# Performance work log

Measured on AMD Instinct MI355X. Metric: run time of the kernel, lower is better.

The kernel has to match this reference:

```python
import jax, jax.numpy as jnp
import numpy as np
from jax import lax

KS = 3
N = KS ** 3  # 27 kernel taps


def setup_inputs() -> dict:
    key = jax.random.key(0)
    k1, k2, k3 = jax.random.split(key, 3)
    B, Cin, Cout, D, H, W = 1, 32, 32, 32, 48, 48
    x = jax.random.normal(k1, (B, Cin, D, H, W), jnp.float32)
    # offset conv: 81 = 3*27 output channels, no bias (nn.Conv3d(..., bias=False))
    w_off = jax.random.normal(k2, (3 * N, Cin, KS, KS, KS), jnp.float32) * 0.01
    # deform conv kernel (bias defaults to None -> no bias)
    w_def = jax.random.normal(k3, (Cout, Cin, KS, KS, KS), jnp.float32) / np.sqrt(Cin * N)
    return {"x": x, "w_off": w_off, "w_def": w_def}


def _deform_block(x, w_off, w_def):
    B, C, D, H, W = x.shape
    dt = x.dtype

    # standard dense offset conv, padding=1
    offsets = lax.conv_general_dilated(
        x, w_off, (1, 1, 1), [(1, 1), (1, 1), (1, 1)],
        dimension_numbers=("NCDHW", "OIDHW", "NCDHW"))
    off = jnp.transpose(offsets, (0, 2, 3, 4, 1))  # (B,D,H,W,3N)
    od, oh, ow = off[..., :N], off[..., N:2 * N], off[..., 2 * N:]

    # zero-pad input (ConstantPad3d(1))
    xp = jnp.pad(x, ((0, 0), (0, 0), (1, 1), (1, 1), (1, 1)))
    Dp, Hp, Wp = D + 2, H + 2, W + 2

    # p_n: kernel grid offsets in (kd,kh,kw) row-major order, matching conv-weight layout
    r = jnp.arange(-(KS // 2), KS // 2 + 1, dtype=dt)
    pn = jnp.stack(jnp.meshgrid(r, r, r, indexing="ij"), 0).reshape(3, N)
    # p_0: centers in padded coordinates (1..D etc.)
    p0d = jnp.arange(1, D + 1, dtype=dt)[:, None, None, None]
    p0h = jnp.arange(1, H + 1, dtype=dt)[None, :, None, None]
    p0w = jnp.arange(1, W + 1, dtype=dt)[None, None, :, None]

    pd = p0d + pn[0] + od  # (B,D,H,W,N) sampling coords
    ph = p0h + pn[1] + oh
    pw = p0w + pn[2] + ow

    # integer corners (detached in original)
    fd = lax.stop_gradient(jnp.floor(pd))
    fh = lax.stop_gradient(jnp.floor(ph))
    fw = lax.stop_gradient(jnp.floor(pw))
    qd0 = jnp.clip(fd, 0, Dp - 1); qd1 = jnp.clip(fd + 1, 0, Dp - 1)
    qh0 = jnp.clip(fh, 0, Hp - 1); qh1 = jnp.clip(fh + 1, 0, Hp - 1)
    qw0 = jnp.clip(fw, 0, Wp - 1); qw1 = jnp.clip(fw + 1, 0, Wp - 1)

    # clip p to valid range (as in reference impl)
    pd = jnp.clip(pd, 0, Dp - 1)
    ph = jnp.clip(ph, 0, Hp - 1)
    pw = jnp.clip(pw, 0, Wp - 1)

    # trilinear weights per axis: g = 1 - |q - p|
    gd0 = 1 + (qd0 - pd); gd1 = 1 - (qd1 - pd)
    gh0 = 1 + (qh0 - ph); gh1 = 1 - (qh1 - ph)
    gw0 = 1 + (qw0 - pw); gw1 = 1 - (qw1 - pw)

    xf = xp.reshape(B, C, Dp * Hp * Wp)

    def gather(idd, ihh, iww):
        lin = ((idd.astype(jnp.int32) * Hp + ihh.astype(jnp.int32)) * Wp
               + iww.astype(jnp.int32)).reshape(B, 1, -1)
        v = jnp.take_along_axis(xf, jnp.broadcast_to(lin, (B, C, lin.shape[-1])), axis=2)
        return v.reshape(B, C, D, H, W, N)

    x_off = jnp.zeros((B, C, D, H, W, N), dt)
    for gd, idd in ((gd0, qd0), (gd1, qd1)):
        for gh, ihh in ((gh0, qh0), (gh1, qh1)):
            for gw, iww in ((gw0, qw0), (gw1, qw1)):
                x_off = x_off + (gd * gh * gw)[:, None] * gather(idd, ihh, iww)

    # stride-ks conv over reshaped x_offset == weighted sum over the N taps
    Cout = w_def.shape[0]
    out = jnp.einsum("bcdhwn,ocn->bodhw", x_off, w_def.reshape(Cout, C, N))
    return out


def reference(x, w_off, w_def):
    return _deform_block(x, w_off, w_def)
```

## Files before the change

### kernel.cpp

```cpp
#include <hip/hip_runtime.h>

typedef __attribute__((ext_vector_type(8))) short  short8;
typedef __attribute__((ext_vector_type(4))) float  f32x4;
typedef __attribute__((ext_vector_type(2))) float  f32x2;

#define CIN 32
#define COUT 32
#define DD 32
#define HH 48
#define WW 48
#define NTAP 27
#define SPATIAL (DD*HH*WW)

#define BP2_ELEMS (27*6*64*8)
#define OFF_WPK   ((size_t)BP2_ELEMS*2)
#define WPK_ELEMS (27*2*64*8)
#define OFF_XT    (OFF_WPK + (size_t)WPK_ELEMS*2)

#define SB0() __builtin_amdgcn_sched_barrier(0)

__device__ __forceinline__ unsigned short f2bf(float f) {
    union { float f; unsigned u; } v; v.f = f;
    unsigned r = v.u + 0x7FFFu + ((v.u >> 16) & 1u);
    return (unsigned short)(r >> 16);
}
__device__ __forceinline__ float bitsf(unsigned u) {
    union { unsigned u; float f; } v; v.u = u; return v.f;
}

__global__ __launch_bounds__(256) void wprep2_kernel(
        const float* __restrict__ w_off, unsigned short* __restrict__ Bp2)
{
    int i = blockIdx.x * 256 + threadIdx.x;
    if (i >= BP2_ELEMS) return;
    int e    = i & 7;
    int lane = (i >> 3) & 63;
    int j    = (i >> 9) % 6;
    int n    = i / (512 * 6);
    int col = lane & 15, kg = lane >> 4;
    int oc = j * 16 + col, c = kg * 8 + e;
    float v = (oc < 81) ? w_off[((size_t)oc * CIN + c) * NTAP + n] : 0.f;
    Bp2[i] = f2bf(v);
}

__global__ __launch_bounds__(256) void wdefprep_kernel(
        const float* __restrict__ w_def, unsigned short* __restrict__ wpk)
{
    int i = blockIdx.x * 256 + threadIdx.x;
    if (i >= WPK_ELEMS) return;
    int e    = i & 7;
    int lane = (i >> 3) & 63;
    int half = (i >> 9) & 1;
    int n    = i >> 10;
    int kg = lane >> 4, col = lane & 15;
    int c  = kg * 8 + e, oc = half * 16 + col;
    wpk[i] = f2bf(w_def[((size_t)oc * CIN + c) * NTAP + n]);
}

__global__ __launch_bounds__(256) void xtrans_kernel(
        const float* __restrict__ x, unsigned short* __restrict__ xT)
{
    __shared__ float t[CIN][65];
    const int p0 = blockIdx.x * 64;
    const int tid = threadIdx.x;
    const int tx = tid & 63, ty = tid >> 6;
    #pragma unroll
    for (int k = 0; k < 8; ++k) {
        int c = ty + k * 4;
        t[c][tx] = x[(size_t)c * SPATIAL + p0 + tx];
    }
    __syncthreads();
    const int pl = tid >> 2, cg = (tid & 3) * 8;
    short8 v;
    #pragma unroll
    for (int i = 0; i < 8; ++i) v[i] = (short)f2bf(t[cg + i][pl]);
    *(short8*)&xT[((size_t)(p0 + pl)) * 32 + cg] = v;
}

struct Gath {
    uint4 cw[8];
    float gg[8];
};

__device__ __forceinline__ void tap_issue(
        Gath& tb, const uint4* __restrict__ Xu,
        float od, float oh, float ow,
        int n, int d, int h, int w, int kg)
{
    float rd = (float)(n / 9) - 1.f;
    float rh = (float)((n / 3) % 3) - 1.f;
    float rw = (float)(n % 3) - 1.f;

    float pdp = (float)(d + 1) + rd + od;
    float php = (float)(h + 1) + rh + oh;
    float pwp = (float)(w + 1) + rw + ow;

    float fd = floorf(pdp), fh = floorf(php), fw = floorf(pwp);
    float qd0 = fminf(fmaxf(fd,       0.f), 33.f);
    float qd1 = fminf(fmaxf(fd + 1.f, 0.f), 33.f);
    float qh0 = fminf(fmaxf(fh,       0.f), 49.f);
    float qh1 = fminf(fmaxf(fh + 1.f, 0.f), 49.f);
    float qw0 = fminf(fmaxf(fw,       0.f), 49.f);
    float qw1 = fminf(fmaxf(fw + 1.f, 0.f), 49.f);
    float pcd = fminf(fmaxf(pdp, 0.f), 33.f);
    float pch = fminf(fmaxf(php, 0.f), 49.f);
    float pcw = fminf(fmaxf(pwp, 0.f), 49.f);

    float gd0 = 1.f + (qd0 - pcd), gd1 = 1.f - (qd1 - pcd);
    float gh0 = 1.f + (qh0 - pch), gh1 = 1.f - (qh1 - pch);
    float gw0 = 1.f + (qw0 - pcw), gw1 = 1.f - (qw1 - pcw);
    gd0 = (qd0 >= 1.f && qd0 <= 32.f) ? gd0 : 0.f;
    gd1 = (qd1 >= 1.f && qd1 <= 32.f) ? gd1 : 0.f;
    gh0 = (qh0 >= 1.f && qh0 <= 48.f) ? gh0 : 0.f;
    gh1 = (qh1 >= 1.f && qh1 <= 48.f) ? gh1 : 0.f;
    gw0 = (qw0 >= 1.f && qw0 <= 48.f) ? gw0 : 0.f;
    gw1 = (qw1 >= 1.f && qw1 <= 48.f) ? gw1 : 0.f;
    int zd0 = (int)fminf(fmaxf(qd0, 1.f), 32.f) - 1;
    int zd1 = (int)fminf(fmaxf(qd1, 1.f), 32.f) - 1;
    int zh0 = (int)fminf(fmaxf(qh0, 1.f), 48.f) - 1;
    int zh1 = (int)fminf(fmaxf(qh1, 1.f), 48.f) - 1;
    int zw0 = (int)fminf(fmaxf(qw0, 1.f), 48.f) - 1;
    int zw1 = (int)fminf(fmaxf(qw1, 1.f), 48.f) - 1;

    int bd0 = zd0 * 2304, bd1 = zd1 * 2304;
    int bh0 = zh0 * 48,   bh1 = zh1 * 48;
    float gdh00 = gd0 * gh0, gdh01 = gd0 * gh1;
    float gdh10 = gd1 * gh0, gdh11 = gd1 * gh1;

    tb.cw[0] = Xu[(size_t)(bd0 + bh0 + zw0) * 4 + kg];
    tb.cw[1] = Xu[(size_t)(bd0 + bh0 + zw1) * 4 + kg];
    tb.cw[2] = Xu[(size_t)(bd0 + bh1 + zw0) * 4 + kg];
    tb.cw[3] = Xu[(size_t)(bd0 + bh1 + zw1) * 4 + kg];
    tb.cw[4] = Xu[(size_t)(bd1 + bh0 + zw0) * 4 + kg];
    tb.cw[5] = Xu[(size_t)(bd1 + bh0 + zw1) * 4 + kg];
    tb.cw[6] = Xu[(size_t)(bd1 + bh1 + zw0) * 4 + kg];
    tb.cw[7] = Xu[(size_t)(bd1 + bh1 + zw1) * 4 + kg];

    tb.gg[0] = gdh00 * gw0;  tb.gg[1] = gdh00 * gw1;
    tb.gg[2] = gdh01 * gw0;  tb.gg[3] = gdh01 * gw1;
    tb.gg[4] = gdh10 * gw0;  tb.gg[5] = gdh10 * gw1;
    tb.gg[6] = gdh11 * gw0;  tb.gg[7] = gdh11 * gw1;
}

__device__ __forceinline__ void tap_consume(
        const Gath& tb, short8 b0, short8 b1, f32x4& acc0, f32x4& acc1)
{
    f32x2 xa0 = {0.f, 0.f}, xa1 = {0.f, 0.f};
    f32x2 xa2 = {0.f, 0.f}, xa3 = {0.f, 0.f};

    #pragma unroll
    for (int e = 0; e < 8; ++e) {
        uint4 cw = tb.cw[e];
        f32x2 g2 = {tb.gg[e], tb.gg[e]};
        f32x2 v0 = {bitsf(cw.x << 16), bitsf(cw.x & 0xFFFF0000u)};
        f32x2 v1 = {bitsf(cw.y << 16), bitsf(cw.y & 0xFFFF0000u)};
        f32x2 v2 = {bitsf(cw.z << 16), bitsf(cw.z & 0xFFFF0000u)};
        f32x2 v3 = {bitsf(cw.w << 16), bitsf(cw.w & 0xFFFF0000u)};
        asm("v_pk_fma_f32 %0, %1, %2, %0" : "+v"(xa0) : "v"(v0), "v"(g2));
        asm("v_pk_fma_f32 %0, %1, %2, %0" : "+v"(xa1) : "v"(v1), "v"(g2));
        asm("v_pk_fma_f32 %0, %1, %2, %0" : "+v"(xa2) : "v"(v2), "v"(g2));
        asm("v_pk_fma_f32 %0, %1, %2, %0" : "+v"(xa3) : "v"(v3), "v"(g2));
    }

    union { unsigned u[4]; short8 s; } av;
    asm("v_cvt_pk_bf16_f32 %0, %1, %2" : "=v"(av.u[0]) : "v"(xa0.x), "v"(xa0.y));
    asm("v_cvt_pk_bf16_f32 %0, %1, %2" : "=v"(av.u[1]) : "v"(xa1.x), "v"(xa1.y));
    asm("v_cvt_pk_bf16_f32 %0, %1, %2" : "=v"(av.u[2]) : "v"(xa2.x), "v"(xa2.y));
    asm("v_cvt_pk_bf16_f32 %0, %1, %2" : "=v"(av.u[3]) : "v"(xa3.x), "v"(xa3.y));

    acc0 = __builtin_amdgcn_mfma_f32_16x16x32_bf16(av.s, b0, acc0, 0, 0, 0);
    acc1 = __builtin_amdgcn_mfma_f32_16x16x32_bf16(av.s, b1, acc1, 0, 0, 0);
}

__global__ __launch_bounds__(128, 2) void fused_deform9(
        const unsigned short* __restrict__ xT,
        const unsigned short* __restrict__ Bp2,
        const unsigned short* __restrict__ wpk,
        float* __restrict__ out)
{
    __shared__ float offl[2][2][16][82];

    const int bid  = (int)blockIdx.x;
    const int sbid = (bid & 7) * 144 + (bid >> 3);

    const int tid  = threadIdx.x;
    const int lane = tid & 63, wv = tid >> 6;
    const int p0   = sbid * 64 + wv * 32;
    const int kg   = lane >> 4;
    const int row  = lane & 15;
    const int pos0 = p0 + row;
    const int pos1 = p0 + 16 + row;
    const int w0c = pos0 % WW, h0c = (pos0 / WW) % HH, d0c = pos0 / (WW * HH);
    const int w1c = pos1 % WW, h1c = (pos1 / WW) % HH, d1c = pos1 / (WW * HH);

    const uint4* Xu = (const uint4*)xT;
    const uint4* Bu = (const uint4*)Bp2;
    const uint4* Wu = (const uint4*)wpk;

    f32x4 cacc0[6], cacc1[6];
    #pragma unroll
    for (int j = 0; j < 6; ++j) {
        cacc0[j] = (f32x4){0.f, 0.f, 0.f, 0.f};
        cacc1[j] = (f32x4){0.f, 0.f, 0.f, 0.f};
    }

    {
        #pragma unroll 1
        for (int n = 0; n < NTAP; ++n) {
            int td = n / 9, th = (n / 3) % 3, tw = n % 3;
            int dis = (td - 1) * 2304 + (th - 1) * 48 + (tw - 1);
            int v0 = ((unsigned)(d0c + td - 1) < DD) & ((unsigned)(h0c + th - 1) < HH)
                   & ((unsigned)(w0c + tw - 1) < WW);
            int v1 = ((unsigned)(d1c + td - 1) < DD) & ((unsigned)(h1c + th - 1) < HH)
                   & ((unsigned)(w1c + tw - 1) < WW);
            uint4 a0 = Xu[(size_t)(v0 ? pos0 + dis : pos0) * 4 + kg];
            uint4 a1 = Xu[(size_t)(v1 ? pos1 + dis : pos1) * 4 + kg];
            uint4 wt[6];
            #pragma unroll
            for (int j = 0; j < 6; ++j)
                wt[j] = Bu[(size_t)(n * 6 + j) * 64 + lane];
            SB0();
            if (!v0) { a0.x = 0; a0.y = 0; a0.z = 0; a0.w = 0; }
            if (!v1) { a1.x = 0; a1.y = 0; a1.z = 0; a1.w = 0; }
            union { uint4 u; short8 s; } av0, av1, b;
            av0.u = a0; av1.u = a1;
            #pragma unroll
            for (int j = 0; j < 6; ++j) {
                b.u = wt[j];
                cacc0[j] = __builtin_amdgcn_mfma_f32_16x16x32_bf16(av0.s, b.s, cacc0[j], 0, 0, 0);
                cacc1[j] = __builtin_amdgcn_mfma_f32_16x16x32_bf16(av1.s, b.s, cacc1[j], 0, 0, 0);
            }
        }
    }

    #pragma unroll
    for (int j = 0; j < 6; ++j) {
        #pragma unroll
        for (int r = 0; r < 4; ++r) {
            int col = j * 16 + row;
            if (col < 81) {
                offl[wv][0][kg * 4 + r][col] = cacc0[j][r];
                offl[wv][1][kg * 4 + r][col] = cacc1[j][r];
            }
        }
    }
    __syncthreads();

    const float* ol0 = &offl[wv][0][row][0];
    const float* ol1 = &offl[wv][1][row][0];

    f32x4 acc00 = {0.f, 0.f, 0.f, 0.f}, acc01 = {0.f, 0.f, 0.f, 0.f};
    f32x4 acc10 = {0.f, 0.f, 0.f, 0.f}, acc11 = {0.f, 0.f, 0.f, 0.f};

    {
        Gath g0, g1;
        #pragma unroll 1
        for (int n = 0; n < NTAP; ++n) {
            uint4 wbu0 = Wu[(size_t)(n * 2 + 0) * 64 + lane];
            uint4 wbu1 = Wu[(size_t)(n * 2 + 1) * 64 + lane];
            tap_issue(g0, Xu, ol0[n], ol0[27 + n], ol0[54 + n], n, d0c, h0c, w0c, kg);
            SB0();
            tap_issue(g1, Xu, ol1[n], ol1[27 + n], ol1[54 + n], n, d1c, h1c, w1c, kg);
            SB0();
            union { uint4 u; short8 s; } b0, b1;
            b0.u = wbu0; b1.u = wbu1;
            tap_consume(g0, b0.s, b1.s, acc00, acc01);
            tap_consume(g1, b0.s, b1.s, acc10, acc11);
        }
    }

    const int pb0 = p0 + kg * 4;
    const int pb1 = p0 + 16 + kg * 4;
    *(f32x4*)&out[(size_t)row        * SPATIAL + pb0] = acc00;
    *(f32x4*)&out[(size_t)(16 + row) * SPATIAL + pb0] = acc01;
    *(f32x4*)&out[(size_t)row        * SPATIAL + pb1] = acc10;
    *(f32x4*)&out[(size_t)(16 + row) * SPATIAL + pb1] = acc11;
}

extern "C" void kernel_launch(void* const* d_in, const int* in_sizes, int n_in,
                              void* d_out, int out_size, void* d_ws, size_t ws_size,
                              hipStream_t stream)
{
    const float* x     = (const float*)d_in[0];
    const float* w_off = (const float*)d_in[1];
    const float* w_def = (const float*)d_in[2];
    float* out = (float*)d_out;

    unsigned short* Bp2 = (unsigned short*)((char*)d_ws);
    unsigned short* wpk = (unsigned short*)((char*)d_ws + OFF_WPK);
    unsigned short* xT  = (unsigned short*)((char*)d_ws + OFF_XT);

    wprep2_kernel<<<(BP2_ELEMS + 255) / 256, 256, 0, stream>>>(w_off, Bp2);
    wdefprep_kernel<<<(WPK_ELEMS + 255) / 256, 256, 0, stream>>>(w_def, wpk);
    xtrans_kernel<<<SPATIAL / 64, 256, 0, stream>>>(x, xT);
    fused_deform9<<<SPATIAL / 64, 128, 0, stream>>>(xT, Bp2, wpk, out);
}
```

Before: 123.9 us.

## Software-pipeline deformable gather taps with rotating triple gather buffers

Restructures the tap loop so the trilinear gathers for the next tap are issued before the current tap's gathered values are consumed by MFMA. Three rotating Gath buffers hide global gather latency behind the blend and MFMA work, and the loop is unrolled by three taps. The last iteration issues a redundant clamped gather for tap 26. In exchange it raises register pressure under the 2-waves launch bound, which could cause spills. The offset-store guard was also hoisted out of the inner loop.

```diff
diff --git a/kernel.cpp b/kernel.cpp
--- a/kernel.cpp
+++ b/kernel.cpp
@@ -172,7 +172,7 @@
     acc1 = __builtin_amdgcn_mfma_f32_16x16x32_bf16(av.s, b1, acc1, 0, 0, 0);
 }
 
-__global__ __launch_bounds__(128, 2) void fused_deform9(
+__global__ __launch_bounds__(128, 2) void fused_deform12(
         const unsigned short* __restrict__ xT,
         const unsigned short* __restrict__ Bp2,
         const unsigned short* __restrict__ wpk,
@@ -235,10 +235,10 @@
 
     #pragma unroll
     for (int j = 0; j < 6; ++j) {
-        #pragma unroll
-        for (int r = 0; r < 4; ++r) {
-            int col = j * 16 + row;
-            if (col < 81) {
+        int col = j * 16 + row;
+        if (col < 81) {
+            #pragma unroll
+            for (int r = 0; r < 4; ++r) {
                 offl[wv][0][kg * 4 + r][col] = cacc0[j][r];
                 offl[wv][1][kg * 4 + r][col] = cacc1[j][r];
             }
@@ -249,23 +249,46 @@
     const float* ol0 = &offl[wv][0][row][0];
     const float* ol1 = &offl[wv][1][row][0];
 
-    f32x4 acc00 = {0.f, 0.f, 0.f, 0.f}, acc01 = {0.f, 0.f, 0.f, 0.f};
-    f32x4 acc10 = {0.f, 0.f, 0.f, 0.f}, acc11 = {0.f, 0.f, 0.f, 0.f};
+    f32x4 acc00 = {0.f,0.f,0.f,0.f}, acc01 = {0.f,0.f,0.f,0.f};
+    f32x4 acc10 = {0.f,0.f,0.f,0.f}, acc11 = {0.f,0.f,0.f,0.f};
 
     {
-        Gath g0, g1;
+        Gath gX, gY, gZ;
+        tap_issue(gX, Xu, ol0[0], ol0[27], ol0[54], 0, d0c, h0c, w0c, kg);
+        SB0();
+        tap_issue(gY, Xu, ol1[0], ol1[27], ol1[54], 0, d1c, h1c, w1c, kg);
+        SB0();
+
         #pragma unroll 1
-        for (int n = 0; n < NTAP; ++n) {
-            uint4 wbu0 = Wu[(size_t)(n * 2 + 0) * 64 + lane];
-            uint4 wbu1 = Wu[(size_t)(n * 2 + 1) * 64 + lane];
-            tap_issue(g0, Xu, ol0[n], ol0[27 + n], ol0[54 + n], n, d0c, h0c, w0c, kg);
-            SB0();
-            tap_issue(g1, Xu, ol1[n], ol1[27 + n], ol1[54 + n], n, d1c, h1c, w1c, kg);
-            SB0();
-            union { uint4 u; short8 s; } b0, b1;
-            b0.u = wbu0; b1.u = wbu1;
-            tap_consume(g0, b0.s, b1.s, acc00, acc01);
-            tap_consume(g1, b0.s, b1.s, acc10, acc11);
+        for (int n = 0; n < NTAP; n += 3) {
+            int n1 = (n + 1 < NTAP) ? n + 1 : NTAP - 1;
+            int n2 = (n + 2 < NTAP) ? n + 2 : NTAP - 1;
+            int n3 = (n + 3 < NTAP) ? n + 3 : NTAP - 1;
+            union { uint4 u; short8 s; } bA0, bA1, bB0, bB1, bC0, bC1;
+            bA0.u = Wu[(size_t)(n * 2 + 0) * 64 + lane];
+            bA1.u = Wu[(size_t)(n * 2 + 1) * 64 + lane];
+            tap_issue(gZ, Xu, ol0[n1], ol0[27 + n1], ol0[54 + n1], n1, d0c, h0c, w0c, kg);
+            SB0();
+            tap_consume(gX, bA0.s, bA1.s, acc00, acc01);
+            tap_issue(gX, Xu, ol1[n1], ol1[27 + n1], ol1[54 + n1], n1, d1c, h1c, w1c, kg);
+            SB0();
+            tap_consume(gY, bA0.s, bA1.s, acc10, acc11);
+            bB0.u = Wu[(size_t)(n1 * 2 + 0) * 64 + lane];
+            bB1.u = Wu[(size_t)(n1 * 2 + 1) * 64 + lane];
+            tap_issue(gY, Xu, ol0[n2], ol0[27 + n2], ol0[54 + n2], n2, d0c, h0c, w0c, kg);
+            SB0();
+            tap_consume(gZ, bB0.s, bB1.s, acc00, acc01);
+            tap_issue(gZ, Xu, ol1[n2], ol1[27 + n2], ol1[54 + n2], n2, d1c, h1c, w1c, kg);
+            SB0();
+            tap_consume(gX, bB0.s, bB1.s, acc10, acc11);
+            bC0.u = Wu[(size_t)(n2 * 2 + 0) * 64 + lane];
+            bC1.u = Wu[(size_t)(n2 * 2 + 1) * 64 + lane];
+            tap_issue(gX, Xu, ol0[n3], ol0[27 + n3], ol0[54 + n3], n3, d0c, h0c, w0c, kg);
+            SB0();
+            tap_consume(gY, bC0.s, bC1.s, acc00, acc01);
+            tap_issue(gY, Xu, ol1[n3], ol1[27 + n3], ol1[54 + n3], n3, d1c, h1c, w1c, kg);
+            SB0();
+            tap_consume(gZ, bC0.s, bC1.s, acc10, acc11);
         }
     }
 
@@ -293,5 +316,5 @@
     wprep2_kernel<<<(BP2_ELEMS + 255) / 256, 256, 0, stream>>>(w_off, Bp2);
     wdefprep_kernel<<<(WPK_ELEMS + 255) / 256, 256, 0, stream>>>(w_def, wpk);
     xtrans_kernel<<<SPATIAL / 64, 256, 0, stream>>>(x, xT);
-    fused_deform9<<<SPATIAL / 64, 128, 0, stream>>>(xT, Bp2, wpk, out);
-}
+    fused_deform12<<<SPATIAL / 64, 128, 0, stream>>>(xT, Bp2, wpk, out);
+}
```

Result: slower. 318.9 us (+157.4%).
